# Optimization experiments

Measured on AMD Instinct MI355X. Metric: run time of the kernel, lower is better.

## Reference

```python
import jax, jax.numpy as jnp
import numpy as np

SIGMA = 1.0


def _rbf_gram(A, B):
    # A: (Tb, N, C), B: (Tb, M, C) -> (Tb, N, M)
    AA = jnp.sum(A * A, axis=2, keepdims=True)          # (Tb, N, 1)
    BB = jnp.sum(B * B, axis=2, keepdims=True)          # (Tb, M, 1)
    d = AA + jnp.swapaxes(BB, 1, 2) - 2.0 * jnp.einsum('bnc,bmc->bnm', A, B)
    return jnp.exp(-d / (2.0 * SIGMA ** 2))


def setup_inputs() -> dict:
    key = jax.random.key(0)
    kx, ky = jax.random.split(key)
    x = jax.random.normal(kx, (512, 128, 16), dtype=jnp.float32)
    y = jax.random.normal(ky, (512, 128, 16), dtype=jnp.float32)
    return {"x": x, "y": y}


def reference(x, y):
    # x, y: (batch, stream, channel)
    x_fds = jnp.concatenate((x[:, :-1, :], x[:, 1:, :]), axis=1)  # (B, 2(T-1), C)
    y_fds = jnp.concatenate((y[:, :-1, :], y[:, 1:, :]), axis=1)
    xf = jnp.transpose(x_fds, (1, 0, 2))  # (2(T-1), B, C)
    yf = jnp.transpose(y_fds, (1, 0, 2))

    N = xf.shape[1]
    Kxx = _rbf_gram(xf, xf)  # (2(T-1), N, N)
    # off-diagonal mean per batch: (sum - trace) / (N*(N-1))
    e_xx = (Kxx.sum(axis=(1, 2)) - jnp.trace(Kxx, axis1=1, axis2=2)) / (N * (N - 1))
    E_k_x1_x2 = e_xx.mean()

    Kxy = _rbf_gram(xf, yf)
    E_k_x_y = Kxy.mean(axis=(1, 2)).mean()

    return E_k_x1_x2 - 2.0 * E_k_x_y
```

## Files before the change

kernel.cpp:

```cpp
#include <hip/hip_runtime.h>


#define LOG2E 1.4426950408889634f
#define SCALE 1.2011224087864498f
#define SD 9

typedef __attribute__((ext_vector_type(8))) __bf16 bf16x8;
typedef __attribute__((ext_vector_type(4))) float floatx4;

union FragU { unsigned int u[4]; bf16x8 v; };

static __device__ __forceinline__ unsigned short bfbits(__bf16 h) {
    union { __bf16 h; unsigned short s; } u; u.h = h; return u.s;
}
static __device__ __forceinline__ unsigned int packhh(__bf16 a, __bf16 b) {
    return (unsigned int)bfbits(a) | ((unsigned int)bfbits(b) << 16);
}
static __device__ __forceinline__ unsigned int packff(float a, float b) {
    return packhh((__bf16)a, (__bf16)b);
}

static __device__ __forceinline__ void split_store(unsigned int* H, unsigned int* L,
                                                   int idx, float4 f) {
    float s0 = f.x * SCALE, s1 = f.y * SCALE, s2 = f.z * SCALE, s3 = f.w * SCALE;
    __bf16 h0 = (__bf16)s0, h1 = (__bf16)s1, h2 = (__bf16)s2, h3 = (__bf16)s3;
    H[idx]     = packhh(h0, h1);
    H[idx + 1] = packhh(h2, h3);
    L[idx]     = packff(s0 - (float)h0, s1 - (float)h1);
    L[idx + 1] = packff(s2 - (float)h2, s3 - (float)h3);
}

__global__ __launch_bounds__(256, 4) void gram_kernel(const float* __restrict__ x,
                                                      const float* __restrict__ y,
                                                      float* __restrict__ part) {
    __shared__ unsigned int XH[256 * SD], XL[256 * SD], YH[256 * SD], YL[256 * SD];
    __shared__ float gxs[256], gys[256];
    __shared__ float sgrow[4][2][16];
    __shared__ float red[8];

    const int bid   = blockIdx.x;
    const int t     = bid >> 3;
    const int strip = (bid >> 1) & 3;
    const int jhalf = bid & 1;
    const int tid   = threadIdx.x;
    const int w     = tid >> 6;
    const int lane  = tid & 63;
    const int quad  = lane >> 4;
    const int l15   = lane & 15;
    const int qh    = quad & 1;

    const float4* __restrict__ x4 = (const float4*)x;
    const float4* __restrict__ y4 = (const float4*)y;
    const int slab4 = t * 4;

    {
        const int r = tid;
        const size_t gbase = (size_t)(jhalf * 256 + r) * 512 + slab4;
        float gnx = 0.f, gny = 0.f;
#pragma unroll
        for (int d = 0; d < 4; ++d) {
            float4 fx = x4[gbase + d];
            float4 fy = y4[gbase + d];
            gnx += fx.x * fx.x + fx.y * fx.y + fx.z * fx.z + fx.w * fx.w;
            gny += fy.x * fy.x + fy.y * fy.y + fy.z * fy.z + fy.w * fy.w;
            split_store(XH, XL, r * SD + 2 * d, fx);
            split_store(YH, YL, r * SD + 2 * d, fy);
        }
        gxs[r] = 0.5f * LOG2E * gnx;
        gys[r] = 0.5f * LOG2E * gny;
    }

    bf16x8 a1f[2], a2f[2];
    float preg[2][4];
    const int abase = strip * 128 + w * 32;
    {
        bf16x8 zv;
#pragma unroll
        for (int j = 0; j < 8; ++j) zv[j] = (__bf16)0.0f;
#pragma unroll
        for (int rt = 0; rt < 2; ++rt) {
            const int row = abase + rt * 16 + l15;
            const size_t gb = (size_t)row * 512 + slab4 + qh * 2;
            float4 f0 = x4[gb], f1 = x4[gb + 1];
            float p = f0.x * f0.x + f0.y * f0.y + f0.z * f0.z + f0.w * f0.w
                    + f1.x * f1.x + f1.y * f1.y + f1.z * f1.z + f1.w * f1.w;
            float n = p + __shfl_xor(p, 16, 64);
            if (quad == 0) sgrow[w][rt][l15] = 0.5f * LOG2E * n;
            float sc[8] = { f0.x * SCALE, f0.y * SCALE, f0.z * SCALE, f0.w * SCALE,
                            f1.x * SCALE, f1.y * SCALE, f1.z * SCALE, f1.w * SCALE };
            bf16x8 hv, lv;
#pragma unroll
            for (int j = 0; j < 8; ++j) {
                __bf16 h = (__bf16)sc[j];
                hv[j] = h;
                lv[j] = (__bf16)(sc[j] - (float)h);
            }
            if (quad < 2) { a1f[rt] = hv; a2f[rt] = hv; }
            else          { a1f[rt] = lv; a2f[rt] = zv; }
        }
    }
    __syncthreads();

#pragma unroll
    for (int rt = 0; rt < 2; ++rt)
#pragma unroll
        for (int r = 0; r < 4; ++r)
            preg[rt][r] = -sgrow[w][rt][quad * 4 + r];

    float sxx[4] = {0.f, 0.f, 0.f, 0.f};
    float sxy[4] = {0.f, 0.f, 0.f, 0.f};

    for (int jt = 0; jt < 16; ++jt) {
        const int jrow = jt * 16 + l15;
        const int rb = jrow * SD + qh * 4;
        FragU bh, bl, ch, cl;
        bh.u[0] = XH[rb]; bh.u[1] = XH[rb + 1]; bh.u[2] = XH[rb + 2]; bh.u[3] = XH[rb + 3];
        bl.u[0] = XL[rb]; bl.u[1] = XL[rb + 1]; bl.u[2] = XL[rb + 2]; bl.u[3] = XL[rb + 3];
        ch.u[0] = YH[rb]; ch.u[1] = YH[rb + 1]; ch.u[2] = YH[rb + 2]; ch.u[3] = YH[rb + 3];
        cl.u[0] = YL[rb]; cl.u[1] = YL[rb + 1]; cl.u[2] = YL[rb + 2]; cl.u[3] = YL[rb + 3];
        const float gcx = gxs[jrow];
        const float gcy = gys[jrow];
#pragma unroll
        for (int rt = 0; rt < 2; ++rt) {
            floatx4 c = {0.f, 0.f, 0.f, 0.f};
            c = __builtin_amdgcn_mfma_f32_16x16x32_bf16(a1f[rt], bh.v, c, 0, 0, 0);
            c = __builtin_amdgcn_mfma_f32_16x16x32_bf16(a2f[rt], bl.v, c, 0, 0, 0);
#pragma unroll
            for (int r = 0; r < 4; ++r)
                sxx[r] += __builtin_amdgcn_exp2f(c[r] + (preg[rt][r] - gcx));
            floatx4 d = {0.f, 0.f, 0.f, 0.f};
            d = __builtin_amdgcn_mfma_f32_16x16x32_bf16(a1f[rt], ch.v, d, 0, 0, 0);
            d = __builtin_amdgcn_mfma_f32_16x16x32_bf16(a2f[rt], cl.v, d, 0, 0, 0);
#pragma unroll
            for (int r = 0; r < 4; ++r)
                sxy[r] += __builtin_amdgcn_exp2f(d[r] + (preg[rt][r] - gcy));
        }
    }

    float txx = (sxx[0] + sxx[1]) + (sxx[2] + sxx[3]);
    float txy = (sxy[0] + sxy[1]) + (sxy[2] + sxy[3]);
    for (int off = 32; off > 0; off >>= 1) {
        txx += __shfl_down(txx, off, 64);
        txy += __shfl_down(txy, off, 64);
    }
    if (lane == 0) { red[w] = txx; red[4 + w] = txy; }
    __syncthreads();
    if (tid == 0) {
        const float wt = (t == 0 || t == 127) ? 1.f : 2.f;
        part[bid]        = wt * (red[0] + red[1] + red[2] + red[3]);
        part[1024 + bid] = wt * (red[4] + red[5] + red[6] + red[7]);
    }
}

__global__ __launch_bounds__(256) void finalize_kernel(const float* __restrict__ part,
                                                       float* __restrict__ out) {
    const int tid = threadIdx.x;
    double vxx = 0.0, vxy = 0.0;
#pragma unroll
    for (int k = 0; k < 4; ++k) {
        vxx += (double)part[tid + 256 * k];
        vxy += (double)part[1024 + tid + 256 * k];
    }
    for (int off = 32; off > 0; off >>= 1) {
        vxx += __shfl_down(vxx, off, 64);
        vxy += __shfl_down(vxy, off, 64);
    }
    __shared__ double red[8];
    const int wid = tid >> 6;
    if ((tid & 63) == 0) { red[wid] = vxx; red[4 + wid] = vxy; }
    __syncthreads();
    if (tid == 0) {
        double sxx = red[0] + red[1] + red[2] + red[3];
        double sxy = red[4] + red[5] + red[6] + red[7];
        double e1 = (sxx - 254.0 * 512.0) / (254.0 * 512.0 * 511.0);
        double e2 = sxy / (254.0 * 512.0 * 512.0);
        out[0] = (float)(e1 - 2.0 * e2);
    }
}

extern "C" void kernel_launch(void* const* d_in, const int* in_sizes, int n_in,
                              void* d_out, int out_size, void* d_ws, size_t ws_size,
                              hipStream_t stream) {
    (void)in_sizes; (void)n_in; (void)out_size; (void)ws_size;
    const float* x = (const float*)d_in[0];
    const float* y = (const float*)d_in[1];
    float* out  = (float*)d_out;
    float* part = (float*)d_ws;

    gram_kernel<<<dim3(1024), dim3(256), 0, stream>>>(x, y, part);
    finalize_kernel<<<dim3(1), dim3(256), 0, stream>>>(part, out);
}
```

Measured before the change: 82.73 us.

## Retile gram blocks to 256x128 and factor exp norms out of inner loop

Each block now covers 256 A rows (4 row tiles per wave) against 128 B columns instead of 128x256, so each wave reuses every loaded B fragment across four MFMA row tiles. The per-element exp argument no longer includes the norms. The column norm factor is precomputed as exp2 and applied with an FMA, and the row norm factor is applied once after the loop. LDS rows are stored with a padded layout that allows 128-bit vector loads and stores. The tradeoff is higher register pressure from 32 accumulators and 8 A fragments, and a possible precision risk from multiplying separate exponentials instead of combining the exponents.

```diff
diff --git a/kernel.cpp b/kernel.cpp
--- a/kernel.cpp
+++ b/kernel.cpp
@@ -3,12 +3,13 @@
 
 #define LOG2E 1.4426950408889634f
 #define SCALE 1.2011224087864498f
-#define SD 9
 
 typedef __attribute__((ext_vector_type(8))) __bf16 bf16x8;
 typedef __attribute__((ext_vector_type(4))) float floatx4;
 
-union FragU { unsigned int u[4]; bf16x8 v; };
+union FragU { uint4 q; unsigned int u[4]; bf16x8 v; };
+
+static __device__ __forceinline__ int off(int n) { return (n << 3) + ((n >> 2) << 2); }
 
 static __device__ __forceinline__ unsigned short bfbits(__bf16 h) {
     union { __bf16 h; unsigned short s; } u; u.h = h; return u.s;
@@ -16,32 +17,19 @@
 static __device__ __forceinline__ unsigned int packhh(__bf16 a, __bf16 b) {
     return (unsigned int)bfbits(a) | ((unsigned int)bfbits(b) << 16);
 }
-static __device__ __forceinline__ unsigned int packff(float a, float b) {
-    return packhh((__bf16)a, (__bf16)b);
-}
-
-static __device__ __forceinline__ void split_store(unsigned int* H, unsigned int* L,
-                                                   int idx, float4 f) {
-    float s0 = f.x * SCALE, s1 = f.y * SCALE, s2 = f.z * SCALE, s3 = f.w * SCALE;
-    __bf16 h0 = (__bf16)s0, h1 = (__bf16)s1, h2 = (__bf16)s2, h3 = (__bf16)s3;
-    H[idx]     = packhh(h0, h1);
-    H[idx + 1] = packhh(h2, h3);
-    L[idx]     = packff(s0 - (float)h0, s1 - (float)h1);
-    L[idx + 1] = packff(s2 - (float)h2, s3 - (float)h3);
-}
 
 __global__ __launch_bounds__(256, 4) void gram_kernel(const float* __restrict__ x,
                                                       const float* __restrict__ y,
                                                       float* __restrict__ part) {
-    __shared__ unsigned int XH[256 * SD], XL[256 * SD], YH[256 * SD], YL[256 * SD];
-    __shared__ float gxs[256], gys[256];
-    __shared__ float sgrow[4][2][16];
+    __shared__ unsigned int XH[1152], XL[1152], YH[1152], YL[1152];
+    __shared__ float csx[128], csy[128];
+    __shared__ float srg[256];
     __shared__ float red[8];
 
     const int bid   = blockIdx.x;
     const int t     = bid >> 3;
-    const int strip = (bid >> 1) & 3;
-    const int jhalf = bid & 1;
+    const int strip = (bid >> 2) & 1;
+    const int jq    = bid & 3;
     const int tid   = threadIdx.x;
     const int w     = tid >> 6;
     const int lane  = tid & 63;
@@ -54,38 +42,53 @@
     const int slab4 = t * 4;
 
     {
-        const int r = tid;
-        const size_t gbase = (size_t)(jhalf * 256 + r) * 512 + slab4;
-        float gnx = 0.f, gny = 0.f;
+        const int half = tid >> 7;
+        const int n    = tid & 127;
+        const float4* __restrict__ src4 = half ? y4 : x4;
+        const size_t gb = (size_t)(jq * 128 + n) * 512 + slab4;
+        float4 f0 = src4[gb], f1 = src4[gb + 1], f2 = src4[gb + 2], f3 = src4[gb + 3];
+        float fs[16] = { f0.x, f0.y, f0.z, f0.w, f1.x, f1.y, f1.z, f1.w,
+                         f2.x, f2.y, f2.z, f2.w, f3.x, f3.y, f3.z, f3.w };
+        float g = 0.f;
+        unsigned int hw[8], lw[8];
 #pragma unroll
-        for (int d = 0; d < 4; ++d) {
-            float4 fx = x4[gbase + d];
-            float4 fy = y4[gbase + d];
-            gnx += fx.x * fx.x + fx.y * fx.y + fx.z * fx.z + fx.w * fx.w;
-            gny += fy.x * fy.x + fy.y * fy.y + fy.z * fy.z + fy.w * fy.w;
-            split_store(XH, XL, r * SD + 2 * d, fx);
-            split_store(YH, YL, r * SD + 2 * d, fy);
+        for (int p = 0; p < 8; ++p) {
+            float s0 = fs[2 * p] * SCALE, s1 = fs[2 * p + 1] * SCALE;
+            g += fs[2 * p] * fs[2 * p] + fs[2 * p + 1] * fs[2 * p + 1];
+            __bf16 h0 = (__bf16)s0, h1 = (__bf16)s1;
+            hw[p] = packhh(h0, h1);
+            lw[p] = packhh((__bf16)(s0 - (float)h0), (__bf16)(s1 - (float)h1));
         }
-        gxs[r] = 0.5f * LOG2E * gnx;
-        gys[r] = 0.5f * LOG2E * gny;
+        unsigned int* __restrict__ H = half ? YH : XH;
+        unsigned int* __restrict__ L = half ? YL : XL;
+        const int o = off(n);
+        *(uint4*)&H[o]     = make_uint4(hw[0], hw[1], hw[2], hw[3]);
+        *(uint4*)&H[o + 4] = make_uint4(hw[4], hw[5], hw[6], hw[7]);
+        *(uint4*)&L[o]     = make_uint4(lw[0], lw[1], lw[2], lw[3]);
+        *(uint4*)&L[o + 4] = make_uint4(lw[4], lw[5], lw[6], lw[7]);
+        float* cs = half ? csy : csx;
+        cs[n] = __builtin_amdgcn_exp2f(-0.5f * LOG2E * g);
+    }
+    {
+        const size_t gb = (size_t)(strip * 256 + tid) * 512 + slab4;
+        float4 f0 = x4[gb], f1 = x4[gb + 1], f2 = x4[gb + 2], f3 = x4[gb + 3];
+        float g = f0.x * f0.x + f0.y * f0.y + f0.z * f0.z + f0.w * f0.w
+                + f1.x * f1.x + f1.y * f1.y + f1.z * f1.z + f1.w * f1.w
+                + f2.x * f2.x + f2.y * f2.y + f2.z * f2.z + f2.w * f2.w
+                + f3.x * f3.x + f3.y * f3.y + f3.z * f3.z + f3.w * f3.w;
+        srg[tid] = 0.5f * LOG2E * g;
     }
 
-    bf16x8 a1f[2], a2f[2];
-    float preg[2][4];
-    const int abase = strip * 128 + w * 32;
+    bf16x8 a1f[4], a2f[4];
     {
         bf16x8 zv;
 #pragma unroll
         for (int j = 0; j < 8; ++j) zv[j] = (__bf16)0.0f;
 #pragma unroll
-        for (int rt = 0; rt < 2; ++rt) {
-            const int row = abase + rt * 16 + l15;
+        for (int rt = 0; rt < 4; ++rt) {
+            const int row = strip * 256 + w * 64 + rt * 16 + l15;
             const size_t gb = (size_t)row * 512 + slab4 + qh * 2;
             float4 f0 = x4[gb], f1 = x4[gb + 1];
-            float p = f0.x * f0.x + f0.y * f0.y + f0.z * f0.z + f0.w * f0.w
-                    + f1.x * f1.x + f1.y * f1.y + f1.z * f1.z + f1.w * f1.w;
-            float n = p + __shfl_xor(p, 16, 64);
-            if (quad == 0) sgrow[w][rt][l15] = 0.5f * LOG2E * n;
             float sc[8] = { f0.x * SCALE, f0.y * SCALE, f0.z * SCALE, f0.w * SCALE,
                             f1.x * SCALE, f1.y * SCALE, f1.z * SCALE, f1.w * SCALE };
             bf16x8 hv, lv;
@@ -95,53 +98,57 @@
                 hv[j] = h;
                 lv[j] = (__bf16)(sc[j] - (float)h);
             }
-            if (quad < 2) { a1f[rt] = hv; a2f[rt] = hv; }
-            else          { a1f[rt] = lv; a2f[rt] = zv; }
+            a1f[rt] = (quad < 2) ? hv : lv;
+            a2f[rt] = (quad < 2) ? hv : zv;
         }
     }
     __syncthreads();
 
+    float sxx[4][4], sxy[4][4];
 #pragma unroll
-    for (int rt = 0; rt < 2; ++rt)
+    for (int rt = 0; rt < 4; ++rt)
 #pragma unroll
-        for (int r = 0; r < 4; ++r)
-            preg[rt][r] = -sgrow[w][rt][quad * 4 + r];
+        for (int r = 0; r < 4; ++r) { sxx[rt][r] = 0.f; sxy[rt][r] = 0.f; }
 
-    float sxx[4] = {0.f, 0.f, 0.f, 0.f};
-    float sxy[4] = {0.f, 0.f, 0.f, 0.f};
-
-    for (int jt = 0; jt < 16; ++jt) {
-        const int jrow = jt * 16 + l15;
-        const int rb = jrow * SD + qh * 4;
+    for (int jt = 0; jt < 8; ++jt) {
+        const int n  = jt * 16 + l15;
+        const int rb = off(n) + qh * 4;
         FragU bh, bl, ch, cl;
-        bh.u[0] = XH[rb]; bh.u[1] = XH[rb + 1]; bh.u[2] = XH[rb + 2]; bh.u[3] = XH[rb + 3];
-        bl.u[0] = XL[rb]; bl.u[1] = XL[rb + 1]; bl.u[2] = XL[rb + 2]; bl.u[3] = XL[rb + 3];
-        ch.u[0] = YH[rb]; ch.u[1] = YH[rb + 1]; ch.u[2] = YH[rb + 2]; ch.u[3] = YH[rb + 3];
-        cl.u[0] = YL[rb]; cl.u[1] = YL[rb + 1]; cl.u[2] = YL[rb + 2]; cl.u[3] = YL[rb + 3];
-        const float gcx = gxs[jrow];
-        const float gcy = gys[jrow];
+        bh.q = *(const uint4*)&XH[rb];
+        bl.q = *(const uint4*)&XL[rb];
+        ch.q = *(const uint4*)&YH[rb];
+        cl.q = *(const uint4*)&YL[rb];
+        const float cx = csx[n];
+        const float cy = csy[n];
 #pragma unroll
-        for (int rt = 0; rt < 2; ++rt) {
+        for (int rt = 0; rt < 4; ++rt) {
             floatx4 c = {0.f, 0.f, 0.f, 0.f};
             c = __builtin_amdgcn_mfma_f32_16x16x32_bf16(a1f[rt], bh.v, c, 0, 0, 0);
             c = __builtin_amdgcn_mfma_f32_16x16x32_bf16(a2f[rt], bl.v, c, 0, 0, 0);
 #pragma unroll
             for (int r = 0; r < 4; ++r)
-                sxx[r] += __builtin_amdgcn_exp2f(c[r] + (preg[rt][r] - gcx));
+                sxx[rt][r] = fmaf(__builtin_amdgcn_exp2f(c[r]), cx, sxx[rt][r]);
             floatx4 d = {0.f, 0.f, 0.f, 0.f};
             d = __builtin_amdgcn_mfma_f32_16x16x32_bf16(a1f[rt], ch.v, d, 0, 0, 0);
             d = __builtin_amdgcn_mfma_f32_16x16x32_bf16(a2f[rt], cl.v, d, 0, 0, 0);
 #pragma unroll
             for (int r = 0; r < 4; ++r)
-                sxy[r] += __builtin_amdgcn_exp2f(d[r] + (preg[rt][r] - gcy));
+                sxy[rt][r] = fmaf(__builtin_amdgcn_exp2f(d[r]), cy, sxy[rt][r]);
         }
     }
 
-    float txx = (sxx[0] + sxx[1]) + (sxx[2] + sxx[3]);
-    float txy = (sxy[0] + sxy[1]) + (sxy[2] + sxy[3]);
-    for (int off = 32; off > 0; off >>= 1) {
-        txx += __shfl_down(txx, off, 64);
-        txy += __shfl_down(txy, off, 64);
+    float txx = 0.f, txy = 0.f;
+#pragma unroll
+    for (int rt = 0; rt < 4; ++rt)
+#pragma unroll
+        for (int r = 0; r < 4; ++r) {
+            const float rs = __builtin_amdgcn_exp2f(-srg[w * 64 + rt * 16 + quad * 4 + r]);
+            txx = fmaf(sxx[rt][r], rs, txx);
+            txy = fmaf(sxy[rt][r], rs, txy);
+        }
+    for (int o = 32; o > 0; o >>= 1) {
+        txx += __shfl_down(txx, o, 64);
+        txy += __shfl_down(txy, o, 64);
     }
     if (lane == 0) { red[w] = txx; red[4 + w] = txy; }
     __syncthreads();
@@ -161,9 +168,9 @@
         vxx += (double)part[tid + 256 * k];
         vxy += (double)part[1024 + tid + 256 * k];
     }
-    for (int off = 32; off > 0; off >>= 1) {
-        vxx += __shfl_down(vxx, off, 64);
-        vxy += __shfl_down(vxy, off, 64);
+    for (int o = 32; o > 0; o >>= 1) {
+        vxx += __shfl_down(vxx, o, 64);
+        vxy += __shfl_down(vxy, o, 64);
     }
     __shared__ double red[8];
     const int wid = tid >> 6;
```

New measurement: 77.51 us. -6.3%, faster.
